# Kernel optimization log

Measured on AMD Instinct MI355X. Metric: run time of the kernel, lower is better.

## Reference

```python
import jax, jax.numpy as jnp
import numpy as np

D_MODEL = 1024
NUM_HEADS = 16
D_K = D_MODEL // NUM_HEADS
B, S = 4, 2048


def setup_inputs() -> dict:
    key = jax.random.key(0)
    ks = jax.random.split(key, 12)
    sc = 1.0 / np.sqrt(D_MODEL)
    inp = {
        "query": jax.random.normal(ks[0], (B, S, D_MODEL), jnp.float32),
        "key": jax.random.normal(ks[1], (B, S, D_MODEL), jnp.float32),
        "value": jax.random.normal(ks[2], (B, S, D_MODEL), jnp.float32),
        # causal mask, broadcast over heads: [B, 1, S, S]
        "mask": jnp.broadcast_to(jnp.tril(jnp.ones((S, S), jnp.bool_)), (B, 1, S, S)),
        "wq": jax.random.normal(ks[3], (D_MODEL, D_MODEL), jnp.float32) * sc,
        "bq": jnp.zeros((D_MODEL,), jnp.float32),
        "wk": jax.random.normal(ks[4], (D_MODEL, D_MODEL), jnp.float32) * sc,
        "bk": jnp.zeros((D_MODEL,), jnp.float32),
        "wv": jax.random.normal(ks[5], (D_MODEL, D_MODEL), jnp.float32) * sc,
        "bv": jnp.zeros((D_MODEL,), jnp.float32),
        "wo": jax.random.normal(ks[6], (D_MODEL, D_MODEL), jnp.float32) * sc,
        "bo": jnp.zeros((D_MODEL,), jnp.float32),
    }
    return inp


def _split_heads(x):
    b, s, _ = x.shape
    return x.reshape(b, s, NUM_HEADS, D_K).transpose(0, 2, 1, 3)  # [B,H,S,Dk]


def reference(query, key, value, mask, wq, bq, wk, bk, wv, bv, wo, bo):
    Q = _split_heads(query @ wq.T + bq)
    K = _split_heads(key @ wk.T + bk)
    V = _split_heads(value @ wv.T + bv)
    scores = jnp.einsum("bhqd,bhkd->bhqk", Q, K) / jnp.sqrt(jnp.float32(D_K))
    scores = jnp.where(mask, scores, jnp.float32(-1e9))  # masked_fill(mask==0, -1e9)
    attn = jax.nn.softmax(scores, axis=-1)  # dropout p=0 (eval)
    out = jnp.einsum("bhqk,bhkd->bhqd", attn, V)
    out = out.transpose(0, 2, 1, 3).reshape(query.shape[0], -1, D_MODEL)
    output = out @ wo.T + bo
    return output, attn
```

## Files before the change

kernel.cpp:

```cpp
#include <hip/hip_runtime.h>

typedef unsigned short u16;
typedef __attribute__((ext_vector_type(8))) short bf16x8;
typedef __attribute__((ext_vector_type(4))) float f32x4;

#define MFMA16(a, b, c) __builtin_amdgcn_mfma_f32_16x16x32_bf16((a), (b), (c), 0, 0, 0)

#define GLL(gp, lp)                                                         \
  __builtin_amdgcn_global_load_lds(                                         \
      (const __attribute__((address_space(1))) void*)(const void*)(gp),     \
      (__attribute__((address_space(3))) void*)(void*)(lp), 16, 0, 0)

__device__ __forceinline__ u16 f2bf(float f) {
  union { float f; unsigned u; } c; c.f = f;
  unsigned r = c.u + 0x7FFFu + ((c.u >> 16) & 1u);
  return (u16)(r >> 16);
}

__global__ __launch_bounds__(256) void cvt_bf16_kernel(
    const float* __restrict__ in, u16* __restrict__ out, int n4) {
  int i = blockIdx.x * 256 + threadIdx.x;
  if (i < n4) {
    float4 v = ((const float4*)in)[i];
    ushort4 o;
    o.x = f2bf(v.x); o.y = f2bf(v.y); o.z = f2bf(v.z); o.w = f2bf(v.w);
    ((ushort4*)out)[i] = o;
  }
}

template <int MODE>
__global__ __launch_bounds__(256) void gemm_bt_kernel(
    const u16* __restrict__ A, const u16* __restrict__ Bw,
    const float* __restrict__ bias, void* __restrict__ Cout) {
  constexpr int Kd = 1024;
  __shared__ u16 sA[128 * 32];
  __shared__ u16 sB[128 * 32];
  const int t = threadIdx.x;
  const int m0 = blockIdx.x * 128;
  const int n0 = blockIdx.y * 128;
  const int w = t >> 6, lane = t & 63, lo = lane & 15, qd = lane >> 4;

  f32x4 acc[4][4];
  for (int i = 0; i < 4; i++)
    for (int j = 0; j < 4; j++) acc[i][j] = (f32x4){0.f, 0.f, 0.f, 0.f};

  const int r0 = t >> 2, q0 = (t & 3) * 8;
  const u16* gA0 = A + (size_t)(m0 + r0) * Kd + q0;
  const u16* gA1 = A + (size_t)(m0 + r0 + 64) * Kd + q0;
  const u16* gB0 = Bw + (size_t)(n0 + r0) * Kd + q0;
  const u16* gB1 = Bw + (size_t)(n0 + r0 + 64) * Kd + q0;
  u16* lA0 = &sA[(t & ~63) * 8];
  u16* lA1 = &sA[((t + 256) & ~63) * 8];
  u16* lB0 = &sB[(t & ~63) * 8];
  u16* lB1 = &sB[((t + 256) & ~63) * 8];

  const int am = (w & 1) * 64, bn = (w >> 1) * 64;

  for (int kb = 0; kb < Kd; kb += 32) {
    GLL(gA0 + kb, lA0);
    GLL(gA1 + kb, lA1);
    GLL(gB0 + kb, lB0);
    GLL(gB1 + kb, lB1);
    __syncthreads();
    bf16x8 af[4], bfv[4];
    for (int i = 0; i < 4; i++)
      af[i] = *(const bf16x8*)&sA[(am + i * 16 + lo) * 32 + qd * 8];
    for (int j = 0; j < 4; j++)
      bfv[j] = *(const bf16x8*)&sB[(bn + j * 16 + lo) * 32 + qd * 8];
    for (int i = 0; i < 4; i++)
      for (int j = 0; j < 4; j++) acc[i][j] = MFMA16(af[i], bfv[j], acc[i][j]);
    __syncthreads();
  }

  for (int i = 0; i < 4; i++)
    for (int j = 0; j < 4; j++) {
      const int n = n0 + bn + j * 16 + lo;
      const float bval = bias[n];
      for (int r = 0; r < 4; r++) {
        const int m = m0 + am + i * 16 + qd * 4 + r;
        float v = acc[i][j][r] + bval;
        if constexpr (MODE == 3) {
          ((float*)Cout)[(size_t)m * 1024 + n] = v;
        } else {
          const int bb = m >> 11, s = m & 2047, h = n >> 6, d = n & 63;
          if constexpr (MODE == 0)
            ((u16*)Cout)[((size_t)(bb * 16 + h) * 2048 + s) * 64 + d] = f2bf(v);
          else
            ((u16*)Cout)[((size_t)(bb * 16 + h) * 64 + d) * 2048 + s] = f2bf(v);
        }
      }
    }
}

__global__ __launch_bounds__(256) void attn_fused_kernel(
    const u16* __restrict__ Q, const u16* __restrict__ K,
    const u16* __restrict__ Vt, float* __restrict__ attn,
    u16* __restrict__ ctx) {
  __shared__ u16 Plds[4][16 * 40];
  const int qt = blockIdx.x, bh = blockIdx.y;
  const int t = threadIdx.x, w = t >> 6, lane = t & 63, lo = lane & 15, qd = lane >> 4;
  const u16* Qh = Q + (size_t)bh * 2048 * 64;
  const u16* Kh = K + (size_t)bh * 2048 * 64;
  const u16* Vh = Vt + (size_t)bh * 64 * 2048;
  float* Ah = attn + (size_t)bh * 2048 * 2048;
  const int qrow0 = qt * 64 + w * 16;
  const float scale2 = 0.125f * 1.44269504088896f;

  bf16x8 aq0 = *(const bf16x8*)&Qh[(qrow0 + lo) * 64 + qd * 8];
  bf16x8 aq1 = *(const bf16x8*)&Qh[(qrow0 + lo) * 64 + 32 + qd * 8];

  float sum4[4] = {0.f, 0.f, 0.f, 0.f};
  const int nkt = (qrow0 + 16) >> 4;
  for (int kt = 0; kt < nkt; ++kt) {
    bf16x8 b0 = *(const bf16x8*)&Kh[(kt * 16 + lo) * 64 + qd * 8];
    bf16x8 b1 = *(const bf16x8*)&Kh[(kt * 16 + lo) * 64 + 32 + qd * 8];
    f32x4 s = (f32x4){0.f, 0.f, 0.f, 0.f};
    s = MFMA16(aq0, b0, s);
    s = MFMA16(aq1, b1, s);
    const int col = kt * 16 + lo;
    for (int r = 0; r < 4; r++) {
      const int row = qrow0 + qd * 4 + r;
      if (col <= row) sum4[r] += exp2f(s[r] * scale2);
    }
  }
  for (int off = 1; off < 16; off <<= 1)
    for (int r = 0; r < 4; r++) sum4[r] += __shfl_xor(sum4[r], off, 64);
  float rinv[4];
  for (int r = 0; r < 4; r++) rinv[r] = 1.f / sum4[r];

  f32x4 oacc[4];
  for (int i = 0; i < 4; i++) oacc[i] = (f32x4){0.f, 0.f, 0.f, 0.f};
  const int kcend = ((qrow0 + 16 + 31) >> 5) << 5;
  u16* Pw = &Plds[w][0];
  for (int kc = 0; kc < kcend; kc += 32) {
    f32x4 st[2];
    for (int tt = 0; tt < 2; ++tt) {
      const int kb = kc + tt * 16;
      bf16x8 b0 = *(const bf16x8*)&Kh[(kb + lo) * 64 + qd * 8];
      bf16x8 b1 = *(const bf16x8*)&Kh[(kb + lo) * 64 + 32 + qd * 8];
      f32x4 s = (f32x4){0.f, 0.f, 0.f, 0.f};
      s = MFMA16(aq0, b0, s);
      s = MFMA16(aq1, b1, s);
      st[tt] = s;
    }
    for (int tt = 0; tt < 2; ++tt)
      for (int r = 0; r < 4; r++) {
        const int col = kc + tt * 16 + lo;
        const int row = qrow0 + qd * 4 + r;
        const float p = (col <= row) ? exp2f(st[tt][r] * scale2) * rinv[r] : 0.f;
        Ah[(size_t)row * 2048 + col] = p;
        Pw[(qd * 4 + r) * 40 + tt * 16 + lo] = f2bf(p);
      }
    bf16x8 pf = *(const bf16x8*)&Pw[lo * 40 + qd * 8];
    for (int d0 = 0; d0 < 4; ++d0) {
      bf16x8 vf = *(const bf16x8*)&Vh[(size_t)(d0 * 16 + lo) * 2048 + kc + qd * 8];
      oacc[d0] = MFMA16(pf, vf, oacc[d0]);
    }
  }

  const float4 z4 = make_float4(0.f, 0.f, 0.f, 0.f);
  for (int r = 0; r < 16; ++r) {
    float* rowp = Ah + (size_t)(qrow0 + r) * 2048;
    for (int c = kcend + lane * 4; c < 2048; c += 256) *(float4*)(rowp + c) = z4;
  }

  const int bb = bh >> 4, h = bh & 15;
  for (int d0 = 0; d0 < 4; ++d0)
    for (int r = 0; r < 4; r++) {
      const int row = qrow0 + qd * 4 + r;
      ctx[(size_t)(bb * 2048 + row) * 1024 + h * 64 + d0 * 16 + lo] =
          f2bf(oacc[d0][r]);
    }
}

extern "C" void kernel_launch(void* const* d_in, const int* in_sizes, int n_in,
                              void* d_out, int out_size, void* d_ws, size_t ws_size,
                              hipStream_t stream) {
  const float* query = (const float*)d_in[0];
  const float* key   = (const float*)d_in[1];
  const float* value = (const float*)d_in[2];
  const float* wq = (const float*)d_in[4];
  const float* bq = (const float*)d_in[5];
  const float* wk = (const float*)d_in[6];
  const float* bk = (const float*)d_in[7];
  const float* wv = (const float*)d_in[8];
  const float* bv = (const float*)d_in[9];
  const float* wo = (const float*)d_in[10];
  const float* bo = (const float*)d_in[11];

  char* ws = (char*)d_ws;
  const size_t MB = 1024 * 1024;
  u16* Xq = (u16*)(ws + 0 * MB);
  u16* Xk = (u16*)(ws + 16 * MB);
  u16* Xv = (u16*)(ws + 32 * MB);
  u16* Wq = (u16*)(ws + 48 * MB);
  u16* Wk = (u16*)(ws + 50 * MB);
  u16* Wv = (u16*)(ws + 52 * MB);
  u16* Wo = (u16*)(ws + 54 * MB);
  u16* Qb = (u16*)(ws + 56 * MB);
  u16* Kb = (u16*)(ws + 72 * MB);
  u16* Vtb = (u16*)(ws + 88 * MB);
  u16* ctx = Xq;

  cvt_bf16_kernel<<<8192, 256, 0, stream>>>(query, Xq, 2097152);
  cvt_bf16_kernel<<<8192, 256, 0, stream>>>(key, Xk, 2097152);
  cvt_bf16_kernel<<<8192, 256, 0, stream>>>(value, Xv, 2097152);
  cvt_bf16_kernel<<<1024, 256, 0, stream>>>(wq, Wq, 262144);
  cvt_bf16_kernel<<<1024, 256, 0, stream>>>(wk, Wk, 262144);
  cvt_bf16_kernel<<<1024, 256, 0, stream>>>(wv, Wv, 262144);
  cvt_bf16_kernel<<<1024, 256, 0, stream>>>(wo, Wo, 262144);

  dim3 gg(64, 8);
  gemm_bt_kernel<0><<<gg, 256, 0, stream>>>(Xq, Wq, bq, Qb);
  gemm_bt_kernel<0><<<gg, 256, 0, stream>>>(Xk, Wk, bk, Kb);
  gemm_bt_kernel<2><<<gg, 256, 0, stream>>>(Xv, Wv, bv, Vtb);

  float* out = (float*)d_out;
  float* attn = out + (size_t)8192 * 1024;
  attn_fused_kernel<<<dim3(32, 64), 256, 0, stream>>>(Qb, Kb, Vtb, attn, ctx);

  gemm_bt_kernel<3><<<gg, 256, 0, stream>>>(ctx, Wo, bo, (void*)out);
}
```

Before: 1.879 ms.

## Swizzle workgroups, stage V-transpose stores via LDS, split upper-triangle zeroing kernel

Remaps block indices in the GEMM and attention kernels so neighbouring workgroups share operand tiles in cache. The V projection now transposes its output tile through shared memory, so each global store is a coalesced 16-byte write instead of a scattered 2-byte one. The attention kernel unrolls the row-sum pass four K tiles at a time and issues V and K loads ahead of the exp work. Zeroing of the masked upper triangle of the attention matrix moves into its own row-parallel kernel, which adds a launch but takes that uneven store work off the causal attention blocks.

```diff
diff --git a/kernel.cpp b/kernel.cpp
--- a/kernel.cpp
+++ b/kernel.cpp
@@ -36,8 +36,10 @@
   __shared__ u16 sA[128 * 32];
   __shared__ u16 sB[128 * 32];
   const int t = threadIdx.x;
-  const int m0 = blockIdx.x * 128;
-  const int n0 = blockIdx.y * 128;
+  const int wg = blockIdx.x + (blockIdx.y << 6);
+  const int swz = ((wg & 7) << 6) | (wg >> 3);
+  const int m0 = (swz >> 3) * 128;
+  const int n0 = (swz & 7) * 128;
   const int w = t >> 6, lane = t & 63, lo = lane & 15, qd = lane >> 4;
 
   f32x4 acc[4][4];
@@ -72,24 +74,57 @@
     __syncthreads();
   }
 
-  for (int i = 0; i < 4; i++)
-    for (int j = 0; j < 4; j++) {
-      const int n = n0 + bn + j * 16 + lo;
-      const float bval = bias[n];
-      for (int r = 0; r < 4; r++) {
-        const int m = m0 + am + i * 16 + qd * 4 + r;
-        float v = acc[i][j][r] + bval;
-        if constexpr (MODE == 3) {
-          ((float*)Cout)[(size_t)m * 1024 + n] = v;
-        } else {
-          const int bb = m >> 11, s = m & 2047, h = n >> 6, d = n & 63;
-          if constexpr (MODE == 0)
+  if constexpr (MODE == 2) {
+    __shared__ u16 sT[64 * 136];
+    const int bb = m0 >> 11;
+    const int s0 = m0 & 2047;
+    const int h0 = n0 >> 6;
+    for (int half = 0; half < 2; ++half) {
+      __syncthreads();
+      if ((w >> 1) == half) {
+        for (int j = 0; j < 4; j++) {
+          const float bval = bias[n0 + half * 64 + j * 16 + lo];
+          for (int i = 0; i < 4; i++)
+            for (int r = 0; r < 4; r++)
+              sT[(j * 16 + lo) * 136 + am + i * 16 + qd * 4 + r] =
+                  f2bf(acc[i][j][r] + bval);
+        }
+      }
+      __syncthreads();
+      const int nr = t >> 2;
+      u16* dst = (u16*)Cout +
+                 ((size_t)((bb * 16 + h0 + half) * 64 + nr)) * 2048 + s0;
+      for (int c = 0; c < 4; ++c) {
+        const int ch = (t & 3) + c * 4;
+        *(uint4*)(dst + ch * 8) = *(const uint4*)(&sT[nr * 136 + ch * 8]);
+      }
+    }
+  } else {
+    for (int i = 0; i < 4; i++)
+      for (int j = 0; j < 4; j++) {
+        const int n = n0 + bn + j * 16 + lo;
+        const float bval = bias[n];
+        for (int r = 0; r < 4; r++) {
+          const int m = m0 + am + i * 16 + qd * 4 + r;
+          float v = acc[i][j][r] + bval;
+          if constexpr (MODE == 3) {
+            ((float*)Cout)[(size_t)m * 1024 + n] = v;
+          } else {
+            const int bb = m >> 11, s = m & 2047, h = n >> 6, d = n & 63;
             ((u16*)Cout)[((size_t)(bb * 16 + h) * 2048 + s) * 64 + d] = f2bf(v);
-          else
-            ((u16*)Cout)[((size_t)(bb * 16 + h) * 64 + d) * 2048 + s] = f2bf(v);
+          }
         }
       }
-    }
+  }
+}
+
+__global__ __launch_bounds__(256) void zero_upper_kernel(float* __restrict__ attn) {
+  const int t = threadIdx.x, w = t >> 6, lane = t & 63;
+  const int row = blockIdx.x * 4 + w;
+  float* rowp = attn + ((size_t)blockIdx.y * 2048 + row) * 2048;
+  const int kz = ((((row >> 4) << 4) + 47) >> 5) << 5;
+  const float4 z4 = make_float4(0.f, 0.f, 0.f, 0.f);
+  for (int c = kz + lane * 4; c < 2048; c += 256) *(float4*)(rowp + c) = z4;
 }
 
 __global__ __launch_bounds__(256) void attn_fused_kernel(
@@ -97,7 +132,9 @@
     const u16* __restrict__ Vt, float* __restrict__ attn,
     u16* __restrict__ ctx) {
   __shared__ u16 Plds[4][16 * 40];
-  const int qt = blockIdx.x, bh = blockIdx.y;
+  const int wg = blockIdx.x + (blockIdx.y << 5);
+  const int swz = ((wg & 7) << 8) | (wg >> 3);
+  const int qt = swz & 31, bh = swz >> 5;
   const int t = threadIdx.x, w = t >> 6, lane = t & 63, lo = lane & 15, qd = lane >> 4;
   const u16* Qh = Q + (size_t)bh * 2048 * 64;
   const u16* Kh = K + (size_t)bh * 2048 * 64;
@@ -110,15 +147,43 @@
   bf16x8 aq1 = *(const bf16x8*)&Qh[(qrow0 + lo) * 64 + 32 + qd * 8];
 
   float sum4[4] = {0.f, 0.f, 0.f, 0.f};
-  const int nkt = (qrow0 + 16) >> 4;
-  for (int kt = 0; kt < nkt; ++kt) {
-    bf16x8 b0 = *(const bf16x8*)&Kh[(kt * 16 + lo) * 64 + qd * 8];
-    bf16x8 b1 = *(const bf16x8*)&Kh[(kt * 16 + lo) * 64 + 32 + qd * 8];
+  const int p1end = qrow0 + 16;
+  const int nfull = p1end >> 6;
+  for (int kc6 = 0; kc6 < nfull; ++kc6) {
+    const int kc = kc6 << 6;
+    bf16x8 b0[4], b1[4];
+#pragma unroll
+    for (int tt = 0; tt < 4; ++tt) {
+      b0[tt] = *(const bf16x8*)&Kh[(kc + tt * 16 + lo) * 64 + qd * 8];
+      b1[tt] = *(const bf16x8*)&Kh[(kc + tt * 16 + lo) * 64 + 32 + qd * 8];
+    }
+    f32x4 st[4];
+#pragma unroll
+    for (int tt = 0; tt < 4; ++tt) {
+      f32x4 s = (f32x4){0.f, 0.f, 0.f, 0.f};
+      s = MFMA16(aq0, b0[tt], s);
+      s = MFMA16(aq1, b1[tt], s);
+      st[tt] = s;
+    }
+#pragma unroll
+    for (int tt = 0; tt < 4; ++tt) {
+      const int col = kc + tt * 16 + lo;
+#pragma unroll
+      for (int r = 0; r < 4; ++r) {
+        const int row = qrow0 + qd * 4 + r;
+        if (col <= row) sum4[r] += exp2f(st[tt][r] * scale2);
+      }
+    }
+  }
+  for (int kb = nfull << 6; kb < p1end; kb += 16) {
+    bf16x8 b0 = *(const bf16x8*)&Kh[(kb + lo) * 64 + qd * 8];
+    bf16x8 b1 = *(const bf16x8*)&Kh[(kb + lo) * 64 + 32 + qd * 8];
     f32x4 s = (f32x4){0.f, 0.f, 0.f, 0.f};
     s = MFMA16(aq0, b0, s);
     s = MFMA16(aq1, b1, s);
-    const int col = kt * 16 + lo;
-    for (int r = 0; r < 4; r++) {
+    const int col = kb + lo;
+#pragma unroll
+    for (int r = 0; r < 4; ++r) {
       const int row = qrow0 + qd * 4 + r;
       if (col <= row) sum4[r] += exp2f(s[r] * scale2);
     }
@@ -133,35 +198,36 @@
   const int kcend = ((qrow0 + 16 + 31) >> 5) << 5;
   u16* Pw = &Plds[w][0];
   for (int kc = 0; kc < kcend; kc += 32) {
-    f32x4 st[2];
-    for (int tt = 0; tt < 2; ++tt) {
-      const int kb = kc + tt * 16;
-      bf16x8 b0 = *(const bf16x8*)&Kh[(kb + lo) * 64 + qd * 8];
-      bf16x8 b1 = *(const bf16x8*)&Kh[(kb + lo) * 64 + 32 + qd * 8];
-      f32x4 s = (f32x4){0.f, 0.f, 0.f, 0.f};
-      s = MFMA16(aq0, b0, s);
-      s = MFMA16(aq1, b1, s);
-      st[tt] = s;
-    }
-    for (int tt = 0; tt < 2; ++tt)
-      for (int r = 0; r < 4; r++) {
-        const int col = kc + tt * 16 + lo;
-        const int row = qrow0 + qd * 4 + r;
-        const float p = (col <= row) ? exp2f(st[tt][r] * scale2) * rinv[r] : 0.f;
-        Ah[(size_t)row * 2048 + col] = p;
-        Pw[(qd * 4 + r) * 40 + tt * 16 + lo] = f2bf(p);
-      }
+    bf16x8 vf0 = *(const bf16x8*)&Vh[(size_t)(0 * 16 + lo) * 2048 + kc + qd * 8];
+    bf16x8 vf1 = *(const bf16x8*)&Vh[(size_t)(1 * 16 + lo) * 2048 + kc + qd * 8];
+    bf16x8 vf2 = *(const bf16x8*)&Vh[(size_t)(2 * 16 + lo) * 2048 + kc + qd * 8];
+    bf16x8 vf3 = *(const bf16x8*)&Vh[(size_t)(3 * 16 + lo) * 2048 + kc + qd * 8];
+    bf16x8 kb00 = *(const bf16x8*)&Kh[(kc + lo) * 64 + qd * 8];
+    bf16x8 kb01 = *(const bf16x8*)&Kh[(kc + lo) * 64 + 32 + qd * 8];
+    bf16x8 kb10 = *(const bf16x8*)&Kh[(kc + 16 + lo) * 64 + qd * 8];
+    bf16x8 kb11 = *(const bf16x8*)&Kh[(kc + 16 + lo) * 64 + 32 + qd * 8];
+    f32x4 s0 = (f32x4){0.f, 0.f, 0.f, 0.f};
+    f32x4 s1 = (f32x4){0.f, 0.f, 0.f, 0.f};
+    s0 = MFMA16(aq0, kb00, s0);
+    s0 = MFMA16(aq1, kb01, s0);
+    s1 = MFMA16(aq0, kb10, s1);
+    s1 = MFMA16(aq1, kb11, s1);
+#pragma unroll
+    for (int r = 0; r < 4; ++r) {
+      const int row = qrow0 + qd * 4 + r;
+      const int c0 = kc + lo, c1 = kc + 16 + lo;
+      const float p0 = (c0 <= row) ? exp2f(s0[r] * scale2) * rinv[r] : 0.f;
+      const float p1 = (c1 <= row) ? exp2f(s1[r] * scale2) * rinv[r] : 0.f;
+      Ah[(size_t)row * 2048 + c0] = p0;
+      Ah[(size_t)row * 2048 + c1] = p1;
+      Pw[(qd * 4 + r) * 40 + lo] = f2bf(p0);
+      Pw[(qd * 4 + r) * 40 + 16 + lo] = f2bf(p1);
+    }
     bf16x8 pf = *(const bf16x8*)&Pw[lo * 40 + qd * 8];
-    for (int d0 = 0; d0 < 4; ++d0) {
-      bf16x8 vf = *(const bf16x8*)&Vh[(size_t)(d0 * 16 + lo) * 2048 + kc + qd * 8];
-      oacc[d0] = MFMA16(pf, vf, oacc[d0]);
-    }
-  }
-
-  const float4 z4 = make_float4(0.f, 0.f, 0.f, 0.f);
-  for (int r = 0; r < 16; ++r) {
-    float* rowp = Ah + (size_t)(qrow0 + r) * 2048;
-    for (int c = kcend + lane * 4; c < 2048; c += 256) *(float4*)(rowp + c) = z4;
+    oacc[0] = MFMA16(pf, vf0, oacc[0]);
+    oacc[1] = MFMA16(pf, vf1, oacc[1]);
+    oacc[2] = MFMA16(pf, vf2, oacc[2]);
+    oacc[3] = MFMA16(pf, vf3, oacc[3]);
   }
 
   const int bb = bh >> 4, h = bh & 15;
@@ -217,6 +283,8 @@
 
   float* out = (float*)d_out;
   float* attn = out + (size_t)8192 * 1024;
+
+  zero_upper_kernel<<<dim3(512, 64), 256, 0, stream>>>(attn);
   attn_fused_kernel<<<dim3(32, 64), 256, 0, stream>>>(Qb, Kb, Vtb, attn, ctx);
 
   gemm_bt_kernel<3><<<gg, 256, 0, stream>>>(ctx, Wo, bo, (void*)out);
```

Measured after the change: 1.787 ms. -4.9%, faster.
